# Kernel optimization log

Measured on AMD Instinct MI355X. Metric: run time of the kernel, lower is better.

## Reference

```python
import jax, jax.numpy as jnp
import numpy as np

H = 8          # num_heads
WIN = 256      # window_size (even); half-window = 128
NEG = -1e30    # stand-in for -inf that keeps softmax grad finite


def setup_inputs() -> dict:
    key = jax.random.key(0)
    ks = jax.random.split(key, 6)
    B, S, D, E = 2, 2048, 512, 512
    x = jax.random.normal(ks[0], (B, S, D), dtype=jnp.float32)
    padding_mask = jax.random.randint(ks[1], (B, S), 0, 2, dtype=jnp.int32)
    Wqkv = jax.random.normal(ks[2], (3 * E, D), dtype=jnp.float32) * 0.02
    bqkv = jnp.zeros((3 * E,), dtype=jnp.float32)
    Wo = jax.random.normal(ks[3], (E, E), dtype=jnp.float32) * 0.02
    bo = jnp.zeros((E,), dtype=jnp.float32)
    return {"x": x, "padding_mask": padding_mask, "Wqkv": Wqkv, "bqkv": bqkv,
            "Wo": Wo, "bo": bo}


def reference(x, padding_mask, Wqkv, bqkv, Wo, bo):
    B, S, _ = x.shape
    E = Wo.shape[0]
    Dh = E // H
    # qkv projection -> [B, H, S, 3*Dh]
    qkv = (x @ Wqkv.T + bqkv).reshape(B, S, H, 3 * Dh).transpose(0, 2, 1, 3)
    q, k, v = jnp.split(qkv, 3, axis=-1)
    # full S x S scores (original materializes [B,H,S,S]); scale by sqrt(head_dim)
    scores = jnp.einsum('bhsd,bhtd->bhst', q, k) / jnp.sqrt(jnp.float32(Dh))
    # sliding-window band: |i - j| <= window_size // 2
    i = jnp.arange(S)[:, None]
    j = jnp.arange(S)[None, :]
    band = jnp.abs(i - j) <= (WIN // 2)               # [S, S]
    # padding: entry valid only if both row and col tokens are non-pad
    pad = padding_mask.astype(bool)                    # [B, S]
    valid = band[None, None] & pad[:, None, None, :] & pad[:, None, :, None]
    scores = jnp.where(valid, scores, NEG)
    A = jax.nn.softmax(scores, axis=-1)
    # rows with no valid entry -> nan_to_num(., 0) in original -> zeros here
    row_valid = jnp.any(valid, axis=-1, keepdims=True)
    A = jnp.where(row_valid, A, 0.0)
    Y = jnp.einsum('bhst,bhtd->bhsd', A, v)            # [B,H,S,Dh]
    Y = Y.transpose(0, 2, 1, 3).reshape(B, S, E)
    return Y @ Wo.T + bo
```

## Files before the change

### kernel.cpp

```cpp
#include <hip/hip_runtime.h>

#define NH   8
#define SEQ  2048
#define DIM  512
#define EMB  512
#define DH   64
#define HALF 128
#define QT   32
#define KW2  288
#define SCS2 292

typedef __attribute__((ext_vector_type(8))) short short8;
typedef __attribute__((ext_vector_type(4))) float f32x4;

__device__ __forceinline__ unsigned short f2bf(float f) {
    unsigned int u = __float_as_uint(f);
    return (unsigned short)((u + 0x7fffu + ((u >> 16) & 1u)) >> 16);
}

__device__ __forceinline__ unsigned cvtpk(float lo, float hi) {
    unsigned r;
    asm("v_cvt_pk_bf16_f32 %0, %1, %2" : "=v"(r) : "v"(lo), "v"(hi));
    return r;
}

__device__ __forceinline__ void gload_lds16(const void* g, void* l) {
    __builtin_amdgcn_global_load_lds((__attribute__((address_space(1))) void*)g,
                                     (__attribute__((address_space(3))) void*)l,
                                     16, 0, 0);
}

__global__ __launch_bounds__(256)
void gemm_qkv(const float* __restrict__ A, const float* __restrict__ B,
              const float* __restrict__ bias, unsigned short* __restrict__ qkvh,
              unsigned short* __restrict__ vT) {
    constexpr int BM = 128, BN = 64, BK = 64;
    __shared__ unsigned short As[BM * BK];
    __shared__ unsigned short Bs[BN * BK];
    const int bid = blockIdx.x;
    const int wg = (bid & 7) * 96 + (bid >> 3);
    const int bm = (wg / 24) * BM, bn = (wg % 24) * BN;
    const int t = threadIdx.x, lane = t & 63, wid = t >> 6;
    const int wr = wid >> 1, wc = wid & 1;
    const int lr = lane & 15, lg = lane >> 4;

    f32x4 acc[4][2];
    #pragma unroll
    for (int m = 0; m < 4; ++m)
        #pragma unroll
        for (int n = 0; n < 2; ++n)
            acc[m][n] = (f32x4){0.f, 0.f, 0.f, 0.f};

    for (int kt = 0; kt < DIM; kt += BK) {
        #pragma unroll
        for (int i = 0; i < 4; ++i) {
            const int c = t + 256 * i, r = c >> 3, c8 = c & 7;
            const float4* src = (const float4*)(A + (size_t)(bm + r) * DIM + kt + c8 * 8);
            const float4 v0 = src[0], v1 = src[1];
            const uint4 pk = make_uint4(cvtpk(v0.x, v0.y), cvtpk(v0.z, v0.w),
                                        cvtpk(v1.x, v1.y), cvtpk(v1.z, v1.w));
            *(uint4*)&As[r * 64 + ((c8 ^ (r & 7)) << 3)] = pk;
        }
        #pragma unroll
        for (int i = 0; i < 2; ++i) {
            const int c = t + 256 * i, r = c >> 3, c8 = c & 7;
            const float4* src = (const float4*)(B + (size_t)(bn + r) * DIM + kt + c8 * 8);
            const float4 v0 = src[0], v1 = src[1];
            const uint4 pk = make_uint4(cvtpk(v0.x, v0.y), cvtpk(v0.z, v0.w),
                                        cvtpk(v1.x, v1.y), cvtpk(v1.z, v1.w));
            *(uint4*)&Bs[r * 64 + ((c8 ^ (r & 7)) << 3)] = pk;
        }
        __syncthreads();
        short8 af[2][4], bf[2][2];
        #pragma unroll
        for (int kk = 0; kk < 2; ++kk) {
            #pragma unroll
            for (int m = 0; m < 4; ++m) {
                const int row = wr * 64 + m * 16 + lr;
                af[kk][m] = *(const short8*)&As[row * 64 + (((kk * 4 + lg) ^ (row & 7)) << 3)];
            }
            #pragma unroll
            for (int n = 0; n < 2; ++n) {
                const int row = wc * 32 + n * 16 + lr;
                bf[kk][n] = *(const short8*)&Bs[row * 64 + (((kk * 4 + lg) ^ (row & 7)) << 3)];
            }
        }
        #pragma unroll
        for (int kk = 0; kk < 2; ++kk)
            #pragma unroll
            for (int m = 0; m < 4; ++m)
                #pragma unroll
                for (int n = 0; n < 2; ++n)
                    acc[m][n] = __builtin_amdgcn_mfma_f32_16x16x32_bf16(af[kk][m], bf[kk][n], acc[m][n], 0, 0, 0);
        __syncthreads();
    }

    unsigned short* Tr = As;
    #pragma unroll
    for (int n = 0; n < 2; ++n) {
        const int cl = wc * 32 + n * 16 + lr;
        const float bv = bias[bn + cl];
        #pragma unroll
        for (int m = 0; m < 4; ++m)
            #pragma unroll
            for (int r = 0; r < 4; ++r)
                Tr[(wr * 64 + m * 16 + lg * 4 + r) * 72 + cl] = f2bf(acc[m][n][r] + bv);
    }
    __syncthreads();

    const int h = bn / 192, ty = (bn >> 6) % 3;
    const int bb = bm >> 11, s0 = bm & 2047;
    if (ty < 2) {
        unsigned short* plane = qkvh + (((size_t)(bb * NH + h) * 3 + ty) * SEQ) * DH;
        const int s = t >> 1, hf = (t & 1) * 32;
        unsigned short* dst = plane + (size_t)(s0 + s) * DH + hf;
        #pragma unroll
        for (int k8 = 0; k8 < 4; ++k8)
            *(short8*)&dst[k8 * 8] = *(const short8*)&Tr[s * 72 + hf + k8 * 8];
    } else {
        const int d = t >> 2, pp = t & 3;
        unsigned short* vrow = vT + ((size_t)(bb * NH + h) * DH + d) * SEQ + s0 + pp * 32;
        #pragma unroll
        for (int k8 = 0; k8 < 4; ++k8) {
            alignas(16) unsigned short tmp[8];
            #pragma unroll
            for (int k = 0; k < 8; ++k) tmp[k] = Tr[(pp * 32 + k8 * 8 + k) * 72 + d];
            *(short8*)&vrow[k8 * 8] = *(short8*)tmp;
        }
    }
}

__global__ __launch_bounds__(256)
void attn_mfma(const unsigned short* __restrict__ qkvh,
               const unsigned short* __restrict__ vT,
               const int* __restrict__ pad,
               unsigned short* __restrict__ Yb) {
    const int bid = blockIdx.x;
    const int wg = (bid & 7) * 128 + (bid >> 3);
    const int bh = wg >> 6, qt = wg & 63;
    const int b = bh >> 3, h = bh & 7;
    const int i0 = qt * QT, kb = i0 - HALF;
    const int t = threadIdx.x, lane = t & 63, w = t >> 6;
    const int lr = lane & 15, lg = lane >> 4;

    __shared__ float Sc[QT * SCS2];

    const unsigned short* Qg = qkvh + ((size_t)bh * 3 + 0) * SEQ * DH;
    const unsigned short* Kg = qkvh + ((size_t)bh * 3 + 1) * SEQ * DH;
    const unsigned short* vTg = vT + (size_t)bh * DH * SEQ;
    const int* padb = pad + b * SEQ;

    short8 qf[2][2];
    #pragma unroll
    for (int half = 0; half < 2; ++half)
        #pragma unroll
        for (int kk = 0; kk < 2; ++kk)
            qf[half][kk] = *(const short8*)&Qg[(size_t)(i0 + half * 16 + lr) * DH + kk * 32 + lg * 8];

    for (int tile = w; tile < 18; tile += 4) {
        const int jl = tile * 16 + lr;
        const int j = kb + jl;
        const int jc = j < 0 ? 0 : (j > SEQ - 1 ? SEQ - 1 : j);
        const int kv = (j >= 0 && j < SEQ) ? padb[j] : 0;
        f32x4 a0 = (f32x4){0.f, 0.f, 0.f, 0.f};
        f32x4 a1 = (f32x4){0.f, 0.f, 0.f, 0.f};
        __builtin_amdgcn_s_setprio(1);
        #pragma unroll
        for (int kk = 0; kk < 2; ++kk) {
            const short8 bfr = *(const short8*)&Kg[(size_t)jc * DH + kk * 32 + lg * 8];
            a0 = __builtin_amdgcn_mfma_f32_16x16x32_bf16(qf[0][kk], bfr, a0, 0, 0, 0);
            a1 = __builtin_amdgcn_mfma_f32_16x16x32_bf16(qf[1][kk], bfr, a1, 0, 0, 0);
        }
        __builtin_amdgcn_s_setprio(0);
        #pragma unroll
        for (int r = 0; r < 4; ++r) {
            const int q0 = lg * 4 + r, q1 = 16 + q0;
            const bool ok0 = kv && (jl >= q0) && (jl <= q0 + 2 * HALF);
            const bool ok1 = kv && (jl >= q1) && (jl <= q1 + 2 * HALF);
            Sc[q0 * SCS2 + jl] = ok0 ? a0[r] * 0.125f : -1e30f;
            Sc[q1 * SCS2 + jl] = ok1 ? a1[r] * 0.125f : -1e30f;
        }
    }
    __syncthreads();

    for (int r = w; r < QT; r += 4) {
        float* row = &Sc[r * SCS2];
        unsigned short* prow = (unsigned short*)row;
        if (!padb[i0 + r]) {
            #pragma unroll
            for (int u = 0; u < 5; ++u) {
                const int jl = lane + 64 * u;
                if (jl < KW2) prow[jl] = 0;
            }
            continue;
        }
        float v[5];
        float mx = -1e30f;
        #pragma unroll
        for (int u = 0; u < 5; ++u) {
            const int jl = lane + 64 * u;
            v[u] = (jl < KW2) ? row[jl] : -1e30f;
            mx = fmaxf(mx, v[u]);
        }
        #pragma unroll
        for (int off = 32; off; off >>= 1) mx = fmaxf(mx, __shfl_xor(mx, off));
        float s = 0.f;
        #pragma unroll
        for (int u = 0; u < 5; ++u) { v[u] = __expf(v[u] - mx); s += v[u]; }
        #pragma unroll
        for (int off = 32; off; off >>= 1) s += __shfl_xor(s, off);
        const float inv = 1.f / s;
        asm volatile("" ::: "memory");
        #pragma unroll
        for (int u = 0; u < 5; ++u) {
            const int jl = lane + 64 * u;
            if (jl < KW2) prow[jl] = f2bf(v[u] * inv);
        }
    }
    __syncthreads();

    f32x4 o0 = (f32x4){0.f, 0.f, 0.f, 0.f};
    f32x4 o1 = (f32x4){0.f, 0.f, 0.f, 0.f};
    const unsigned short* PbU = (const unsigned short*)Sc;
    const int d0 = w * 16 + lr;
    #pragma unroll
    for (int c = 0; c < 9; ++c) {
        int j0 = kb + c * 32 + lg * 8;
        j0 = j0 < 0 ? 0 : (j0 > SEQ - 8 ? SEQ - 8 : j0);
        const short8 vf  = *(const short8*)&vTg[(size_t)d0 * SEQ + j0];
        const short8 pf0 = *(const short8*)&PbU[lr * (SCS2 * 2) + c * 32 + lg * 8];
        const short8 pf1 = *(const short8*)&PbU[(16 + lr) * (SCS2 * 2) + c * 32 + lg * 8];
        __builtin_amdgcn_s_setprio(1);
        o0 = __builtin_amdgcn_mfma_f32_16x16x32_bf16(pf0, vf, o0, 0, 0, 0);
        o1 = __builtin_amdgcn_mfma_f32_16x16x32_bf16(pf1, vf, o1, 0, 0, 0);
        __builtin_amdgcn_s_setprio(0);
    }

    #pragma unroll
    for (int r = 0; r < 4; ++r) {
        Yb[(size_t)(b * SEQ + i0 + lg * 4 + r) * EMB + h * DH + d0]      = f2bf(o0[r]);
        Yb[(size_t)(b * SEQ + i0 + 16 + lg * 4 + r) * EMB + h * DH + d0] = f2bf(o1[r]);
    }
}

__global__ __launch_bounds__(256)
void gemm_out(const unsigned short* __restrict__ A, const float* __restrict__ B,
              const float* __restrict__ bias, float* __restrict__ C) {
    constexpr int BM = 64, BN = 64, BK = 64;
    __shared__ unsigned short As[BM * BK];
    __shared__ unsigned short Bs[BN * BK];
    const int bid = blockIdx.x;
    const int wg = (bid & 7) * 64 + (bid >> 3);
    const int bm = (wg >> 3) * BM, bn = (wg & 7) * BN;
    const int t = threadIdx.x, lane = t & 63, wid = t >> 6;
    const int wr = wid >> 1, wc = wid & 1;
    const int lr = lane & 15, lg = lane >> 4;

    f32x4 acc[2][2];
    #pragma unroll
    for (int m = 0; m < 2; ++m)
        #pragma unroll
        for (int n = 0; n < 2; ++n)
            acc[m][n] = (f32x4){0.f, 0.f, 0.f, 0.f};

    for (int kt = 0; kt < DIM; kt += BK) {
        #pragma unroll
        for (int off = 0; off < BM * BK; off += 2048) {
            const int e = off + t * 8, r = e >> 6, c4 = (e & 63) >> 3;
            const int gc = (c4 ^ (r & 7)) << 3;
            gload_lds16(A + (size_t)(bm + r) * EMB + kt + gc, &As[e]);
        }
        #pragma unroll
        for (int i = 0; i < 2; ++i) {
            const int c = t + 256 * i, r = c >> 3, c8 = c & 7;
            const float4* src = (const float4*)(B + (size_t)(bn + r) * DIM + kt + c8 * 8);
            const float4 v0 = src[0], v1 = src[1];
            const uint4 pk = make_uint4(cvtpk(v0.x, v0.y), cvtpk(v0.z, v0.w),
                                        cvtpk(v1.x, v1.y), cvtpk(v1.z, v1.w));
            *(uint4*)&Bs[r * 64 + ((c8 ^ (r & 7)) << 3)] = pk;
        }
        __syncthreads();
        short8 af[2][2], bf[2][2];
        #pragma unroll
        for (int kk = 0; kk < 2; ++kk) {
            #pragma unroll
            for (int m = 0; m < 2; ++m) {
                const int row = wr * 32 + m * 16 + lr;
                af[kk][m] = *(const short8*)&As[row * BK + (((kk * 4 + lg) ^ (row & 7)) << 3)];
            }
            #pragma unroll
            for (int n = 0; n < 2; ++n) {
                const int row = wc * 32 + n * 16 + lr;
                bf[kk][n] = *(const short8*)&Bs[row * BK + (((kk * 4 + lg) ^ (row & 7)) << 3)];
            }
        }
        #pragma unroll
        for (int kk = 0; kk < 2; ++kk)
            #pragma unroll
            for (int m = 0; m < 2; ++m)
                #pragma unroll
                for (int n = 0; n < 2; ++n)
                    acc[m][n] = __builtin_amdgcn_mfma_f32_16x16x32_bf16(af[kk][m], bf[kk][n], acc[m][n], 0, 0, 0);
        __syncthreads();
    }

    const int orow = bm + wr * 32 + lg * 4;
    const int oc0 = bn + wc * 32 + lr;
    #pragma unroll
    for (int m = 0; m < 2; ++m)
        #pragma unroll
        for (int n = 0; n < 2; ++n) {
            const int col = oc0 + n * 16;
            const float bv = bias[col];
            #pragma unroll
            for (int r = 0; r < 4; ++r)
                C[(size_t)(orow + m * 16 + r) * EMB + col] = acc[m][n][r] + bv;
        }
}

extern "C" void kernel_launch(void* const* d_in, const int* in_sizes, int n_in,
                              void* d_out, int out_size, void* d_ws, size_t ws_size,
                              hipStream_t stream) {
    const float* x    = (const float*)d_in[0];
    const int*   pad  = (const int*)d_in[1];
    const float* Wqkv = (const float*)d_in[2];
    const float* bqkv = (const float*)d_in[3];
    const float* Wo   = (const float*)d_in[4];
    const float* bo   = (const float*)d_in[5];
    float* out = (float*)d_out;

    char* p = (char*)d_ws;
    unsigned short* qkvh = (unsigned short*)p;
    unsigned short* vT   = (unsigned short*)(p + 12582912);
    unsigned short* Yb   = (unsigned short*)(p + 16777216);

    dim3 blk(256);
    gemm_qkv<<<dim3(768), blk, 0, stream>>>(x, Wqkv, bqkv, qkvh, vT);
    attn_mfma<<<dim3(1024), blk, 0, stream>>>(qkvh, vT, pad, Yb);
    gemm_out<<<dim3(512), blk, 0, stream>>>(Yb, Wo, bo, out);
}
```

Measured before the change: 51.77 us.

## Pre-convert inputs and weights to bf16, load GEMM tiles via direct global-to-LDS

Adds a separate conversion kernel that turns x, Wqkv and Wo from fp32 into bf16 in workspace. Both GEMMs then fill their LDS tiles with swizzled global_load_lds copies instead of loading fp32 into registers, converting and storing. This removes redundant per-tile conversion work (x is re-read by 24 column blocks) and halves GEMM tile traffic. In exchange it adds a kernel launch and an extra full read and write pass over x and the weights.

Result: faster. 48.91 us (-5.5%).

```diff
diff --git a/kernel.cpp b/kernel.cpp
--- a/kernel.cpp
+++ b/kernel.cpp
@@ -18,12 +18,6 @@
     return (unsigned short)((u + 0x7fffu + ((u >> 16) & 1u)) >> 16);
 }
 
-__device__ __forceinline__ unsigned cvtpk(float lo, float hi) {
-    unsigned r;
-    asm("v_cvt_pk_bf16_f32 %0, %1, %2" : "=v"(r) : "v"(lo), "v"(hi));
-    return r;
-}
-
 __device__ __forceinline__ void gload_lds16(const void* g, void* l) {
     __builtin_amdgcn_global_load_lds((__attribute__((address_space(1))) void*)g,
                                      (__attribute__((address_space(3))) void*)l,
@@ -31,7 +25,20 @@
 }
 
 __global__ __launch_bounds__(256)
-void gemm_qkv(const float* __restrict__ A, const float* __restrict__ B,
+void cvt_all(const float* __restrict__ x, const float* __restrict__ wqkv,
+             const float* __restrict__ wo, unsigned short* __restrict__ out) {
+    const int i = blockIdx.x * 256 + threadIdx.x;
+    const float* src;
+    int base;
+    if (i < 524288)      { src = x;    base = 0; }
+    else if (i < 720896) { src = wqkv; base = 524288; }
+    else                 { src = wo;   base = 720896; }
+    float4 v = ((const float4*)src)[i - base];
+    ((ushort4*)out)[i] = make_ushort4(f2bf(v.x), f2bf(v.y), f2bf(v.z), f2bf(v.w));
+}
+
+__global__ __launch_bounds__(256)
+void gemm_qkv(const unsigned short* __restrict__ A, const unsigned short* __restrict__ B,
               const float* __restrict__ bias, unsigned short* __restrict__ qkvh,
               unsigned short* __restrict__ vT) {
     constexpr int BM = 128, BN = 64, BK = 64;
@@ -53,22 +60,16 @@
 
     for (int kt = 0; kt < DIM; kt += BK) {
         #pragma unroll
-        for (int i = 0; i < 4; ++i) {
-            const int c = t + 256 * i, r = c >> 3, c8 = c & 7;
-            const float4* src = (const float4*)(A + (size_t)(bm + r) * DIM + kt + c8 * 8);
-            const float4 v0 = src[0], v1 = src[1];
-            const uint4 pk = make_uint4(cvtpk(v0.x, v0.y), cvtpk(v0.z, v0.w),
-                                        cvtpk(v1.x, v1.y), cvtpk(v1.z, v1.w));
-            *(uint4*)&As[r * 64 + ((c8 ^ (r & 7)) << 3)] = pk;
-        }
-        #pragma unroll
-        for (int i = 0; i < 2; ++i) {
-            const int c = t + 256 * i, r = c >> 3, c8 = c & 7;
-            const float4* src = (const float4*)(B + (size_t)(bn + r) * DIM + kt + c8 * 8);
-            const float4 v0 = src[0], v1 = src[1];
-            const uint4 pk = make_uint4(cvtpk(v0.x, v0.y), cvtpk(v0.z, v0.w),
-                                        cvtpk(v1.x, v1.y), cvtpk(v1.z, v1.w));
-            *(uint4*)&Bs[r * 64 + ((c8 ^ (r & 7)) << 3)] = pk;
+        for (int off = 0; off < BM * BK; off += 2048) {
+            const int e = off + t * 8, r = e >> 6, c4 = (e & 63) >> 3;
+            const int gc = (c4 ^ (r & 7)) << 3;
+            gload_lds16(A + (size_t)(bm + r) * DIM + kt + gc, &As[e]);
+        }
+        #pragma unroll
+        for (int off = 0; off < BN * BK; off += 2048) {
+            const int e = off + t * 8, r = e >> 6, c4 = (e & 63) >> 3;
+            const int gc = (c4 ^ (r & 7)) << 3;
+            gload_lds16(B + (size_t)(bn + r) * DIM + kt + gc, &Bs[e]);
         }
         __syncthreads();
         short8 af[2][4], bf[2][2];
@@ -244,7 +245,7 @@
 }
 
 __global__ __launch_bounds__(256)
-void gemm_out(const unsigned short* __restrict__ A, const float* __restrict__ B,
+void gemm_out(const unsigned short* __restrict__ A, const unsigned short* __restrict__ B,
               const float* __restrict__ bias, float* __restrict__ C) {
     constexpr int BM = 64, BN = 64, BK = 64;
     __shared__ unsigned short As[BM * BK];
@@ -271,13 +272,10 @@
             gload_lds16(A + (size_t)(bm + r) * EMB + kt + gc, &As[e]);
         }
         #pragma unroll
-        for (int i = 0; i < 2; ++i) {
-            const int c = t + 256 * i, r = c >> 3, c8 = c & 7;
-            const float4* src = (const float4*)(B + (size_t)(bn + r) * DIM + kt + c8 * 8);
-            const float4 v0 = src[0], v1 = src[1];
-            const uint4 pk = make_uint4(cvtpk(v0.x, v0.y), cvtpk(v0.z, v0.w),
-                                        cvtpk(v1.x, v1.y), cvtpk(v1.z, v1.w));
-            *(uint4*)&Bs[r * 64 + ((c8 ^ (r & 7)) << 3)] = pk;
+        for (int off = 0; off < BN * BK; off += 2048) {
+            const int e = off + t * 8, r = e >> 6, c4 = (e & 63) >> 3;
+            const int gc = (c4 ^ (r & 7)) << 3;
+            gload_lds16(B + (size_t)(bn + r) * DIM + kt + gc, &Bs[e]);
         }
         __syncthreads();
         short8 af[2][2], bf[2][2];
@@ -330,12 +328,17 @@
     float* out = (float*)d_out;
 
     char* p = (char*)d_ws;
-    unsigned short* qkvh = (unsigned short*)p;
-    unsigned short* vT   = (unsigned short*)(p + 12582912);
-    unsigned short* Yb   = (unsigned short*)(p + 16777216);
+    unsigned short* qkvh  = (unsigned short*)p;
+    unsigned short* vT    = (unsigned short*)(p + 12582912);
+    unsigned short* Yb    = (unsigned short*)(p + 16777216);
+    unsigned short* cvtb  = (unsigned short*)(p + 20971520);
+    unsigned short* xb    = cvtb;
+    unsigned short* wqkvb = cvtb + 2097152;
+    unsigned short* wob   = cvtb + 2883584;
 
     dim3 blk(256);
-    gemm_qkv<<<dim3(768), blk, 0, stream>>>(x, Wqkv, bqkv, qkvh, vT);
+    cvt_all<<<dim3(3072), blk, 0, stream>>>(x, Wqkv, Wo, cvtb);
+    gemm_qkv<<<dim3(768), blk, 0, stream>>>(xb, wqkvb, bqkv, qkvh, vT);
     attn_mfma<<<dim3(1024), blk, 0, stream>>>(qkvh, vT, pad, Yb);
-    gemm_out<<<dim3(512), blk, 0, stream>>>(Yb, Wo, bo, out);
-}
+    gemm_out<<<dim3(512), blk, 0, stream>>>(Yb, wob, bo, out);
+}
```
